# Kernel optimization log

Hardware: AMD Instinct MI355X
Metric: run time of the kernel (lower is better)

The kernel has to match this reference:

```python
import jax, jax.numpy as jnp
import numpy as np

B, N, T = 1, 4096, 512
WQ, HK = 32, 128
ATOM_S, ATOM_Z, TOKEN_S, TOKEN_Z = 128, 16, 384, 128
FEAT = 3 + 1 + 128 + 4 * 64  # 388


def _indexing_matrix(K, Wq, Hk):
    # faithful port of get_indexing_matrix: one-hot banded gather matrix [2K, K*h]
    h = Hk // (Wq // 2)
    ar = jnp.arange(2 * K)
    idx = jnp.clip(ar[None, :] - ar[:, None] + h // 2, 0, h + 1)
    idx = idx.reshape(K, 2, 2 * K)[:, 0, :]                 # [K, 2K]
    oh = jax.nn.one_hot(idx, h + 2, dtype=jnp.float32)[..., 1:-1]  # [K, 2K, h]
    return jnp.transpose(oh, (1, 0, 2)).reshape(2 * K, K * h)


def _to_keys(x, M, Wq, Hk):
    b, n, d = x.shape
    k = n // Wq
    x = x.reshape(b, 2 * k, Wq // 2, d)
    return jnp.einsum('bjid,jk->bkid', x, M).reshape(b, k, Hk, d)


def _ln(x, g, b, eps=1e-5):
    m = jnp.mean(x, axis=-1, keepdims=True)
    v = jnp.var(x, axis=-1, keepdims=True)
    return (x - m) * jax.lax.rsqrt(v + eps) * g + b


def setup_inputs() -> dict:
    key = jax.random.key(0)
    ks = jax.random.split(key, 24)
    s = 0.02
    tok_idx = jnp.sort(jax.random.randint(ks[0], (B, N), 0, T), axis=-1)
    return {
        'ref_pos': jax.random.normal(ks[1], (B, N, 3), jnp.float32),
        'ref_charge': jax.random.normal(ks[2], (B, N), jnp.float32),
        'ref_element': jax.random.uniform(ks[3], (B, N, 128), jnp.float32),
        'ref_atom_name_chars': jax.random.uniform(ks[4], (B, N, 4, 64), jnp.float32),
        'atom_pad_mask': jnp.ones((B, N), dtype=bool),
        'ref_space_uid': jnp.sort(jax.random.randint(ks[5], (B, N), 0, 512), axis=-1),
        'atom_to_token': jax.nn.one_hot(tok_idx, T, dtype=jnp.float32),
        's_trunk': jax.random.normal(ks[6], (B, T, TOKEN_S), jnp.float32),
        'z': jax.random.normal(ks[7], (B, T, T, TOKEN_Z), jnp.float32),
        # learned params, stored [in, out] so y = x @ W (+ b)
        'W_feat': jax.random.normal(ks[8], (FEAT, ATOM_S), jnp.float32) * s,
        'b_feat': jnp.zeros((ATOM_S,), jnp.float32),
        'W_pos': jax.random.normal(ks[9], (3, ATOM_Z), jnp.float32) * s,
        'W_dist': jax.random.normal(ks[10], (1, ATOM_Z), jnp.float32) * s,
        'W_mask': jax.random.normal(ks[11], (1, ATOM_Z), jnp.float32) * s,
        'ln_s_g': jnp.ones((TOKEN_S,), jnp.float32),
        'ln_s_b': jnp.zeros((TOKEN_S,), jnp.float32),
        'W_s2c': jax.random.normal(ks[12], (TOKEN_S, ATOM_S), jnp.float32) * s,
        'ln_z_g': jnp.ones((TOKEN_Z,), jnp.float32),
        'ln_z_b': jnp.zeros((TOKEN_Z,), jnp.float32),
        'W_z2p': jax.random.normal(ks[13], (TOKEN_Z, ATOM_Z), jnp.float32) * s,
        'W_cq': jax.random.normal(ks[14], (ATOM_S, ATOM_Z), jnp.float32) * s,
        'W_ck': jax.random.normal(ks[15], (ATOM_S, ATOM_Z), jnp.float32) * s,
        'W_m1': jax.random.normal(ks[16], (ATOM_Z, ATOM_Z), jnp.float32) * s,
        'W_m2': jax.random.normal(ks[17], (ATOM_Z, ATOM_Z), jnp.float32) * s,
        'W_m3': jax.random.normal(ks[18], (ATOM_Z, ATOM_Z), jnp.float32) * s,
    }


def reference(ref_pos, ref_charge, ref_element, ref_atom_name_chars, atom_pad_mask,
              ref_space_uid, atom_to_token, s_trunk, z,
              W_feat, b_feat, W_pos, W_dist, W_mask,
              ln_s_g, ln_s_b, W_s2c, ln_z_g, ln_z_b, W_z2p,
              W_cq, W_ck, W_m1, W_m2, W_m3):
    b, n, _ = ref_pos.shape
    k = n // WQ
    atom_feats = jnp.concatenate(
        [ref_pos, ref_charge[..., None], ref_element,
         ref_atom_name_chars.reshape(b, n, 4 * 64)], axis=-1)
    c = atom_feats @ W_feat + b_feat                       # [B,N,atom_s]
    q = c
    M = _indexing_matrix(k, WQ, HK)
    tk = lambda x: _to_keys(x, M, WQ, HK)

    pos_q = ref_pos.reshape(b, k, WQ, 1, 3)
    pos_k = tk(ref_pos).reshape(b, k, 1, HK, 3)
    d = pos_k - pos_q                                      # [B,K,W,H,3]
    d_norm = 1.0 / (1.0 + jnp.sum(d * d, axis=-1, keepdims=True))

    mq = atom_pad_mask.reshape(b, k, WQ, 1)
    mk = tk(atom_pad_mask[..., None].astype(jnp.float32)).reshape(b, k, 1, HK) > 0.5
    uq = ref_space_uid.reshape(b, k, WQ, 1)
    uk = tk(ref_space_uid[..., None].astype(jnp.float32)).reshape(b, k, 1, HK).astype(ref_space_uid.dtype)
    v = (mq & mk & (uq == uk)).astype(jnp.float32)[..., None]  # [B,K,W,H,1]

    p = (d @ W_pos) * v
    p = p + (d_norm @ W_dist) * v
    p = p + (v @ W_mask) * v

    # structure_prediction branch
    s2c = _ln(s_trunk, ln_s_g, ln_s_b) @ W_s2c             # [B,T,atom_s]
    c = c + jnp.einsum('bnt,btd->bnd', atom_to_token, s2c)
    a2t_q = atom_to_token.reshape(b, k, WQ, -1)            # [B,K,W,T]
    a2t_k = tk(atom_to_token)                              # [B,K,H,T]
    zp = _ln(z, ln_z_g, ln_z_b) @ W_z2p                    # [B,T,T,atom_z]
    tmp = jnp.einsum('bwki,bijd->bwkjd', a2t_q, zp)        # [B,K,W,T,atom_z]
    p = p + jnp.einsum('bwkjd,bwlj->bwkld', tmp, a2t_k)    # [B,K,W,H,atom_z]

    p = p + jax.nn.relu(c).reshape(b, k, WQ, 1, -1) @ W_cq
    p = p + jax.nn.relu(tk(c)).reshape(b, k, 1, HK, -1) @ W_ck

    h1 = jax.nn.relu(p) @ W_m1
    h2 = jax.nn.relu(h1) @ W_m2
    p = p + jax.nn.relu(h2) @ W_m3
    return (q, c, p)
```

## Files before the change

kernel.cpp:

```cpp
#include <hip/hip_runtime.h>

#define N_ATOMS 4096
#define T_TOK   512
#define TOKEN_S 384
#define TOKEN_Z 128

using bfrag = __attribute__((ext_vector_type(8))) short;
using f4    = __attribute__((ext_vector_type(4))) float;

__device__ __forceinline__ short f2bf(float f) {
    unsigned u = __float_as_uint(f);
    unsigned r = u + 0x7FFFu + ((u >> 16) & 1u);
    return (short)(r >> 16);
}
__device__ __forceinline__ float bf2f(unsigned short s) {
    return __uint_as_float(((unsigned)s) << 16);
}

__global__ __launch_bounds__(256) void setup_kernel(
    const float* __restrict__ a2t, const float* __restrict__ Wz,
    const float* __restrict__ gz, const float* __restrict__ bz,
    const float* __restrict__ Wf, const float* __restrict__ Wcq,
    const float* __restrict__ Wck, const float* __restrict__ Ws2c,
    const float* __restrict__ gs, const float* __restrict__ bs,
    int* __restrict__ tok, short* __restrict__ zpW,
    short* __restrict__ featW, short* __restrict__ WcqF,
    short* __restrict__ WckF, short* __restrict__ s2cW,
    float* __restrict__ bias16, float* __restrict__ cs16,
    float* __restrict__ cs128, float* __restrict__ bs128) {
    const int b = blockIdx.x, tid = threadIdx.x;
    if (b >= 53) {
        const int wave = tid >> 6, lane = tid & 63;
        const int n = (b - 53) * 4 + wave;
        const float* row = a2t + (size_t)n * T_TOK;
        int found = 0;
#pragma unroll
        for (int m = 0; m < T_TOK / 64; ++m)
            if (row[lane + 64 * m] > 0.5f) found = lane + 64 * m;
#pragma unroll
        for (int off = 32; off >= 1; off >>= 1)
            found = max(found, __shfl_xor(found, off, 64));
        if (lane == 0) tok[n] = found;
        return;
    }
    if (b == 51) {
        const int o = tid >> 3, s = tid & 7;
        const float* vec = (o < 16) ? bz : gz;
        const int n = o & 15;
        float p = 0.f;
#pragma unroll
        for (int i = 0; i < 16; ++i) {
            const int k = s + 8 * i;
            p += vec[k] * Wz[k * 16 + n];
        }
        p += __shfl_xor(p, 1, 64); p += __shfl_xor(p, 2, 64);
        p += __shfl_xor(p, 4, 64);
        if (s == 0) { if (o < 16) bias16[n] = p; else cs16[n] = p; }
        return;
    }
    if (b == 52) {
        const int o = tid & 127, arr = tid >> 7;
        const float* vec = arr ? bs : gs;
        float s = 0.f;
        for (int k = 0; k < TOKEN_S; ++k)
            s += vec[k] * Ws2c[(size_t)k * 128 + o];
        if (arr) bs128[o] = s; else cs128[o] = s;
        return;
    }
    const int id = b * 256 + tid;
    const int lane = id & 63, fs = id >> 6;
    const int quad = lane >> 4, n = lane & 15;
    short v[8];
    short* dst;
    if (fs < 4) {
#pragma unroll
        for (int j = 0; j < 8; ++j) {
            int k = fs * 32 + quad * 8 + j;
            v[j] = f2bf(gz[k] * Wz[k * 16 + n]);
        }
        dst = zpW + (size_t)(fs * 64 + lane) * 8;
    } else if (fs < 100) {
        const int idx = fs - 4, kb = idx >> 3, nt = idx & 7;
#pragma unroll
        for (int j = 0; j < 8; ++j) {
            int f = 4 + kb * 32 + quad * 8 + j;
            v[j] = f2bf(Wf[(size_t)f * 128 + nt * 16 + n]);
        }
        dst = featW + (size_t)(idx * 64 + lane) * 8;
    } else if (fs < 104) {
        const int kb = fs - 100;
#pragma unroll
        for (int j = 0; j < 8; ++j) {
            int k = kb * 32 + quad * 8 + j;
            v[j] = f2bf(Wcq[k * 16 + n]);
        }
        dst = WcqF + (size_t)(kb * 64 + lane) * 8;
    } else if (fs < 108) {
        const int kb = fs - 104;
#pragma unroll
        for (int j = 0; j < 8; ++j) {
            int k = kb * 32 + quad * 8 + j;
            v[j] = f2bf(Wck[k * 16 + n]);
        }
        dst = WckF + (size_t)(kb * 64 + lane) * 8;
    } else {
        const int idx = fs - 108, kb = idx >> 3, nt = idx & 7;
#pragma unroll
        for (int j = 0; j < 8; ++j) {
            int k = kb * 32 + quad * 8 + j;
            v[j] = f2bf(gs[k] * Ws2c[(size_t)k * 128 + nt * 16 + n]);
        }
        dst = s2cW + (size_t)(idx * 64 + lane) * 8;
    }
#pragma unroll
    for (int j = 0; j < 8; ++j) dst[j] = v[j];
}

__global__ __launch_bounds__(256) void s2c_mfma_kernel(
    const float* __restrict__ s_trunk, const short* __restrict__ s2cW,
    const float* __restrict__ cs128, const float* __restrict__ bs128,
    float* __restrict__ s2c) {
    const int wave = threadIdx.x >> 6, lane = threadIdx.x & 63;
    const int m = lane & 15, quad = lane >> 4;
    const int wg = blockIdx.x * 4 + wave;
    const int tile = wg >> 3, nt = wg & 7;
    const int t0 = tile * 16;
    const float* xrow = s_trunk + (size_t)(t0 + m) * TOKEN_S;

    bfrag A[12];
    float xs = 0.f, xq = 0.f;
#pragma unroll
    for (int kb = 0; kb < 12; ++kb) {
        const float4* p = (const float4*)(xrow + kb * 32 + quad * 8);
        float4 x0 = p[0], x1 = p[1];
        const float xv[8] = {x0.x, x0.y, x0.z, x0.w, x1.x, x1.y, x1.z, x1.w};
#pragma unroll
        for (int j = 0; j < 8; ++j) {
            A[kb][j] = f2bf(xv[j]);
            xs += xv[j]; xq = fmaf(xv[j], xv[j], xq);
        }
    }
    xs += __shfl_xor(xs, 16, 64); xs += __shfl_xor(xs, 32, 64);
    xq += __shfl_xor(xq, 16, 64); xq += __shfl_xor(xq, 32, 64);
    const float mean = xs * (1.f / TOKEN_S);
    const float var  = xq * (1.f / TOKEN_S) - mean * mean;
    const float rstd = rsqrtf(var + 1e-5f);
    const float mrs  = mean * rstd;

    const bfrag* Bb = (const bfrag*)s2cW;
    f4 acc = {0.f, 0.f, 0.f, 0.f};
#pragma unroll
    for (int kb = 0; kb < 12; ++kb)
        acc = __builtin_amdgcn_mfma_f32_16x16x32_bf16(
            A[kb], Bb[(kb * 8 + nt) * 64 + lane], acc, 0, 0, 0);

    const int cn = nt * 16 + m;
    const float csn = cs128[cn], bsn = bs128[cn];
#pragma unroll
    for (int reg = 0; reg < 4; ++reg) {
        const int r = quad * 4 + reg;
        const float rs = __shfl(rstd, r, 64);
        const float ms = __shfl(mrs, r, 64);
        s2c[(size_t)(t0 + r) * 128 + cn] = rs * acc[reg] - ms * csn + bsn;
    }
}

__global__ __launch_bounds__(256) void zp_mfma_kernel(
    const float* __restrict__ z, const short* __restrict__ zpW,
    const float* __restrict__ bias16, const float* __restrict__ cs16,
    unsigned short* __restrict__ zp_bf) {
    const int wave = threadIdx.x >> 6, lane = threadIdx.x & 63;
    const int m = lane & 15, quad = lane >> 4;
    const size_t r0 = ((size_t)blockIdx.x * 4 + wave) * 16;
    const float* zrow = z + (r0 + m) * (size_t)TOKEN_Z;

    bfrag A[4];
    float xs = 0.f, xq = 0.f;
#pragma unroll
    for (int kb = 0; kb < 4; ++kb) {
        const float4* p = (const float4*)(zrow + kb * 32 + quad * 8);
        float4 x0 = p[0], x1 = p[1];
        const float xv[8] = {x0.x, x0.y, x0.z, x0.w, x1.x, x1.y, x1.z, x1.w};
#pragma unroll
        for (int j = 0; j < 8; ++j) {
            A[kb][j] = f2bf(xv[j]);
            xs += xv[j]; xq = fmaf(xv[j], xv[j], xq);
        }
    }
    xs += __shfl_xor(xs, 16, 64); xs += __shfl_xor(xs, 32, 64);
    xq += __shfl_xor(xq, 16, 64); xq += __shfl_xor(xq, 32, 64);
    const float mean = xs * (1.f / TOKEN_Z);
    const float var  = xq * (1.f / TOKEN_Z) - mean * mean;
    const float rstd = rsqrtf(var + 1e-5f);
    const float mrs  = mean * rstd;

    const bfrag* wb = (const bfrag*)zpW;
    f4 acc = {0.f, 0.f, 0.f, 0.f};
#pragma unroll
    for (int kb = 0; kb < 4; ++kb)
        acc = __builtin_amdgcn_mfma_f32_16x16x32_bf16(A[kb], wb[kb * 64 + lane],
                                                      acc, 0, 0, 0);
    const float csn = cs16[m], bn = bias16[m];
#pragma unroll
    for (int reg = 0; reg < 4; ++reg) {
        const int r = quad * 4 + reg;
        const float rs = __shfl(rstd, r, 64);
        const float ms = __shfl(mrs, r, 64);
        zp_bf[(r0 + r) * 16 + m] =
            (unsigned short)f2bf(rs * acc[reg] - ms * csn + bn);
    }
}

__global__ __launch_bounds__(128) void featcatk_kernel(
    const float* __restrict__ pos, const float* __restrict__ charge,
    const float* __restrict__ elem, const float* __restrict__ namec,
    const float* __restrict__ Wf, const float* __restrict__ bf,
    const float* __restrict__ s2c, const int* __restrict__ tok,
    const short* __restrict__ featW, const short* __restrict__ WcqF,
    const short* __restrict__ WckF, float* __restrict__ q_out,
    float* __restrict__ c_out, float* __restrict__ acq,
    float* __restrict__ ack) {
    __shared__ short ctile[16 * 136];
    const int wave = threadIdx.x >> 6, lane = threadIdx.x & 63;
    const int m = lane & 15, quad = lane >> 4;
    const int a0 = blockIdx.x * 16;
    const int ntb = wave * 4;

    f4 acc[4];
#pragma unroll
    for (int nt = 0; nt < 4; ++nt) acc[nt] = (f4){0.f, 0.f, 0.f, 0.f};
    const bfrag* Bb = (const bfrag*)featW;
#pragma unroll
    for (int kb = 0; kb < 12; ++kb) {
        const int f0 = kb * 32 + quad * 8;
        const float* src = (kb < 4)
            ? (elem + (size_t)(a0 + m) * 128 + f0)
            : (namec + (size_t)(a0 + m) * 256 + f0 - 128);
        float4 x0 = ((const float4*)src)[0];
        float4 x1 = ((const float4*)src)[1];
        bfrag A;
        A[0] = f2bf(x0.x); A[1] = f2bf(x0.y); A[2] = f2bf(x0.z); A[3] = f2bf(x0.w);
        A[4] = f2bf(x1.x); A[5] = f2bf(x1.y); A[6] = f2bf(x1.z); A[7] = f2bf(x1.w);
#pragma unroll
        for (int nt = 0; nt < 4; ++nt)
            acc[nt] = __builtin_amdgcn_mfma_f32_16x16x32_bf16(
                A, Bb[(kb * 8 + ntb + nt) * 64 + lane], acc[nt], 0, 0, 0);
    }
    float px[4], py[4], pz[4], ch[4];
    int tk4[4];
#pragma unroll
    for (int reg = 0; reg < 4; ++reg) {
        const int a = a0 + quad * 4 + reg;
        px[reg] = pos[a * 3 + 0]; py[reg] = pos[a * 3 + 1];
        pz[reg] = pos[a * 3 + 2]; ch[reg] = charge[a];
        tk4[reg] = tok[a];
    }
#pragma unroll
    for (int nt = 0; nt < 4; ++nt) {
        const int cn = (ntb + nt) * 16 + m;
        const float w0 = Wf[cn], w1 = Wf[128 + cn], w2 = Wf[256 + cn],
                    w3 = Wf[384 + cn], bv = bf[cn];
#pragma unroll
        for (int reg = 0; reg < 4; ++reg) {
            const int r = quad * 4 + reg;
            float qv = acc[nt][reg] + px[reg] * w0 + py[reg] * w1 +
                       pz[reg] * w2 + ch[reg] * w3 + bv;
            q_out[(size_t)(a0 + r) * 128 + cn] = qv;
            float cv = qv + s2c[(size_t)tk4[reg] * 128 + cn];
            c_out[(size_t)(a0 + r) * 128 + cn] = cv;
            ctile[r * 136 + cn] = f2bf(fmaxf(cv, 0.f));
        }
    }
    __syncthreads();
    const bfrag* BW = wave ? (const bfrag*)WckF : (const bfrag*)WcqF;
    float* dst = wave ? ack : acq;
    f4 a2 = {0.f, 0.f, 0.f, 0.f};
#pragma unroll
    for (int kb = 0; kb < 4; ++kb) {
        bfrag Af = *(const bfrag*)&ctile[m * 136 + kb * 32 + quad * 8];
        a2 = __builtin_amdgcn_mfma_f32_16x16x32_bf16(Af, BW[kb * 64 + lane],
                                                     a2, 0, 0, 0);
    }
#pragma unroll
    for (int reg = 0; reg < 4; ++reg)
        dst[(size_t)(a0 + quad * 4 + reg) * 16 + m] = a2[reg];
}

__global__ __launch_bounds__(256) void pair_mfma_kernel(
    const float* __restrict__ pos, const int* __restrict__ uid,
    const int* __restrict__ tok, const unsigned short* __restrict__ zp_bf,
    const float* __restrict__ acq, const float* __restrict__ ack,
    const float* __restrict__ W_pos, const float* __restrict__ W_dist,
    const float* __restrict__ W_mask, const float* __restrict__ W_m1,
    const float* __restrict__ W_m2, const float* __restrict__ W_m3,
    float* __restrict__ p_out) {
    const int wave = threadIdx.x >> 6, lane = threadIdx.x & 63;
    const int m = lane & 15, quad = lane >> 4;
    const int qa = blockIdx.x * 4 + wave;
    const int j = qa >> 5;

    bfrag A1, A2, A3;
#pragma unroll
    for (int jj = 0; jj < 4; ++jj) {
        const int d = quad * 4 + jj;
        A1[jj] = f2bf(W_m1[d * 16 + m]); A1[jj + 4] = 0;
        A2[jj] = f2bf(W_m2[d * 16 + m]); A2[jj + 4] = 0;
        A3[jj] = f2bf(W_m3[d * 16 + m]); A3[jj + 4] = 0;
    }
    float wp0[4], wp1[4], wp2[4], wd[4], wm[4];
#pragma unroll
    for (int jj = 0; jj < 4; ++jj) {
        const int d = quad * 4 + jj;
        wp0[jj] = W_pos[d]; wp1[jj] = W_pos[16 + d]; wp2[jj] = W_pos[32 + d];
        wd[jj] = W_dist[d]; wm[jj] = W_mask[d];
    }
    const float pqx = pos[qa * 3 + 0], pqy = pos[qa * 3 + 1],
                pqz = pos[qa * 3 + 2];
    const int uq = uid[qa], tq = tok[qa];
    const float4 aq = *(const float4*)(acq + (size_t)qa * 16 + quad * 4);
    const float aqv[4] = {aq.x, aq.y, aq.z, aq.w};
    float* pbase = p_out + (size_t)qa * 2048;

    const f4 zero = {0.f, 0.f, 0.f, 0.f};
#pragma unroll
    for (int g = 0; g < 8; ++g) {
        const int kk = g * 16 + m;
        const int src = j * 32 + kk - 48;
        const bool valid = ((unsigned)src < (unsigned)N_ATOMS);
        float dx = 0.f, dy = 0.f, dz = 0.f, dn = 0.f, vflag = 0.f;
        float zv[4] = {0.f, 0.f, 0.f, 0.f}, av[4] = {0.f, 0.f, 0.f, 0.f};
        if (valid) {
            dx = pos[src * 3 + 0] - pqx;
            dy = pos[src * 3 + 1] - pqy;
            dz = pos[src * 3 + 2] - pqz;
            dn = 1.f / (1.f + dx * dx + dy * dy + dz * dz);
            vflag = (uid[src] == uq) ? 1.f : 0.f;
            const int tk_ = tok[src];
            ushort4 zl = *(const ushort4*)(zp_bf +
                            ((size_t)tq * 512 + tk_) * 16 + quad * 4);
            float4 al = *(const float4*)(ack + (size_t)src * 16 + quad * 4);
            zv[0] = bf2f(zl.x); zv[1] = bf2f(zl.y);
            zv[2] = bf2f(zl.z); zv[3] = bf2f(zl.w);
            av[0] = al.x; av[1] = al.y; av[2] = al.z; av[3] = al.w;
        }
        float pb[4];
        bfrag B;
#pragma unroll
        for (int jj = 0; jj < 4; ++jj) {
            float t = dx * wp0[jj] + dy * wp1[jj] + dz * wp2[jj] +
                      dn * wd[jj] + wm[jj];
            pb[jj] = vflag * t + zv[jj] + av[jj] + aqv[jj];
            B[jj] = f2bf(fmaxf(pb[jj], 0.f));
            B[jj + 4] = 0;
        }
        f4 t1 = __builtin_amdgcn_mfma_f32_16x16x32_bf16(A1, B, zero, 0, 0, 0);
        bfrag B2;
#pragma unroll
        for (int jj = 0; jj < 4; ++jj) {
            B2[jj] = f2bf(fmaxf(t1[jj], 0.f)); B2[jj + 4] = 0;
        }
        f4 t2 = __builtin_amdgcn_mfma_f32_16x16x32_bf16(A2, B2, zero, 0, 0, 0);
        bfrag B3;
#pragma unroll
        for (int jj = 0; jj < 4; ++jj) {
            B3[jj] = f2bf(fmaxf(t2[jj], 0.f)); B3[jj + 4] = 0;
        }
        f4 t3 = __builtin_amdgcn_mfma_f32_16x16x32_bf16(A3, B3, zero, 0, 0, 0);
        float4 o = make_float4(pb[0] + t3[0], pb[1] + t3[1],
                               pb[2] + t3[2], pb[3] + t3[3]);
        *(float4*)(pbase + kk * 16 + quad * 4) = o;
    }
}

extern "C" void kernel_launch(void* const* d_in, const int* in_sizes, int n_in,
                              void* d_out, int out_size, void* d_ws, size_t ws_size,
                              hipStream_t stream) {
    const float* ref_pos     = (const float*)d_in[0];
    const float* ref_charge  = (const float*)d_in[1];
    const float* ref_element = (const float*)d_in[2];
    const float* ref_name    = (const float*)d_in[3];
    const int*   uid         = (const int*)d_in[5];
    const float* a2t         = (const float*)d_in[6];
    const float* s_trunk     = (const float*)d_in[7];
    const float* z           = (const float*)d_in[8];
    const float* W_feat      = (const float*)d_in[9];
    const float* b_feat      = (const float*)d_in[10];
    const float* W_pos       = (const float*)d_in[11];
    const float* W_dist      = (const float*)d_in[12];
    const float* W_mask      = (const float*)d_in[13];
    const float* ln_s_g      = (const float*)d_in[14];
    const float* ln_s_b      = (const float*)d_in[15];
    const float* W_s2c       = (const float*)d_in[16];
    const float* ln_z_g      = (const float*)d_in[17];
    const float* ln_z_b      = (const float*)d_in[18];
    const float* W_z2p       = (const float*)d_in[19];
    const float* W_cq        = (const float*)d_in[20];
    const float* W_ck        = (const float*)d_in[21];
    const float* W_m1        = (const float*)d_in[22];
    const float* W_m2        = (const float*)d_in[23];
    const float* W_m3        = (const float*)d_in[24];

    float* out = (float*)d_out;
    float* q_out = out;
    float* c_out = out + 524288;
    float* p_out = out + 1048576;

    char* w = (char*)d_ws;
    unsigned short* zp_bf = (unsigned short*)w;
    float* s2c  = (float*)(w + 8388608);
    float* acq  = s2c + 65536;
    float* ack  = acq + 65536;
    int*   tok  = (int*)(ack + 65536);
    short* zpW   = (short*)(tok + 4096);
    short* featW = zpW + 2048;
    short* WcqF  = featW + 49152;
    short* WckF  = WcqF + 2048;
    short* s2cW  = WckF + 2048;
    float* bias16 = (float*)(s2cW + 49152);
    float* cs16   = bias16 + 16;
    float* cs128  = cs16 + 16;
    float* bs128  = cs128 + 128;

    setup_kernel<<<1077, 256, 0, stream>>>(a2t, W_z2p, ln_z_g, ln_z_b,
                                           W_feat, W_cq, W_ck, W_s2c,
                                           ln_s_g, ln_s_b, tok, zpW, featW,
                                           WcqF, WckF, s2cW, bias16, cs16,
                                           cs128, bs128);
    s2c_mfma_kernel<<<64, 256, 0, stream>>>(s_trunk, s2cW, cs128, bs128, s2c);
    zp_mfma_kernel<<<4096, 256, 0, stream>>>(z, zpW, bias16, cs16, zp_bf);
    featcatk_kernel<<<256, 128, 0, stream>>>(ref_pos, ref_charge, ref_element,
                                             ref_name, W_feat, b_feat, s2c, tok,
                                             featW, WcqF, WckF,
                                             q_out, c_out, acq, ack);
    pair_mfma_kernel<<<1024, 256, 0, stream>>>(ref_pos, uid, tok, zp_bf,
                                               acq, ack, W_pos, W_dist, W_mask,
                                               W_m1, W_m2, W_m3, p_out);
}
```

Before: 293.3 us.

## Compute zp projection only for token pairs reachable within atom window band

Builds per-query-token bounds on the key tokens its atoms can attend to (window of ±79 atoms), turns them into a worklist of 16-token tiles, and runs the z layernorm+projection only over those tiles instead of all 512x512 token pairs. This cuts most of the reading of the 128 MB z tensor. It relies on atom_to_token being sorted so the band is contiguous, and it adds small extra kernels and atomics.

```diff
diff --git a/kernel.cpp b/kernel.cpp
--- a/kernel.cpp
+++ b/kernel.cpp
@@ -27,7 +27,8 @@
     short* __restrict__ featW, short* __restrict__ WcqF,
     short* __restrict__ WckF, short* __restrict__ s2cW,
     float* __restrict__ bias16, float* __restrict__ cs16,
-    float* __restrict__ cs128, float* __restrict__ bs128) {
+    float* __restrict__ cs128, float* __restrict__ bs128,
+    int* __restrict__ lo, int* __restrict__ hi) {
     const int b = blockIdx.x, tid = threadIdx.x;
     if (b >= 53) {
         const int wave = tid >> 6, lane = tid & 63;
@@ -59,6 +60,8 @@
         return;
     }
     if (b == 52) {
+        lo[tid] = 0x7FFFFFFF; lo[tid + 256] = 0x7FFFFFFF;
+        hi[tid] = -1;         hi[tid + 256] = -1;
         const int o = tid & 127, arr = tid >> 7;
         const float* vec = arr ? bs : gs;
         float s = 0.f;
@@ -114,6 +117,40 @@
     }
 #pragma unroll
     for (int j = 0; j < 8; ++j) dst[j] = v[j];
+}
+
+__global__ __launch_bounds__(256) void band_kernel(
+    const int* __restrict__ tok, int* __restrict__ lo, int* __restrict__ hi) {
+    const int a = blockIdx.x * 256 + threadIdx.x;
+    const int t = tok[a];
+    int am = a - 79; if (am < 0) am = 0;
+    int ap = a + 79; if (ap > N_ATOMS - 1) ap = N_ATOMS - 1;
+    atomicMin(&lo[t], tok[am]);
+    atomicMax(&hi[t], tok[ap]);
+}
+
+__global__ __launch_bounds__(512) void worklist_kernel(
+    const int* __restrict__ lo, const int* __restrict__ hi,
+    int* __restrict__ wl, int* __restrict__ wl_count) {
+    __shared__ int scan[512];
+    const int t = threadIdx.x;
+    const int l = lo[t], h = hi[t];
+    const int n = (h >= l) ? ((h - l) >> 4) + 1 : 0;
+    scan[t] = n;
+    __syncthreads();
+    for (int off = 1; off < 512; off <<= 1) {
+        int add = (t >= off) ? scan[t - off] : 0;
+        __syncthreads();
+        scan[t] += add;
+        __syncthreads();
+    }
+    const int off0 = scan[t] - n;
+    for (int i = 0; i < n; ++i) {
+        int tk0 = l + i * 16;
+        if (tk0 > T_TOK - 16) tk0 = T_TOK - 16;
+        wl[off0 + i] = (t << 16) | tk0;
+    }
+    if (t == 511) *wl_count = scan[511];
 }
 
 __global__ __launch_bounds__(256) void s2c_mfma_kernel(
@@ -165,49 +202,58 @@
     }
 }
 
-__global__ __launch_bounds__(256) void zp_mfma_kernel(
+__global__ __launch_bounds__(256) void zp_wl_kernel(
     const float* __restrict__ z, const short* __restrict__ zpW,
     const float* __restrict__ bias16, const float* __restrict__ cs16,
+    const int* __restrict__ wl, const int* __restrict__ wl_count,
     unsigned short* __restrict__ zp_bf) {
     const int wave = threadIdx.x >> 6, lane = threadIdx.x & 63;
     const int m = lane & 15, quad = lane >> 4;
-    const size_t r0 = ((size_t)blockIdx.x * 4 + wave) * 16;
-    const float* zrow = z + (r0 + m) * (size_t)TOKEN_Z;
-
-    bfrag A[4];
-    float xs = 0.f, xq = 0.f;
-#pragma unroll
-    for (int kb = 0; kb < 4; ++kb) {
-        const float4* p = (const float4*)(zrow + kb * 32 + quad * 8);
-        float4 x0 = p[0], x1 = p[1];
-        const float xv[8] = {x0.x, x0.y, x0.z, x0.w, x1.x, x1.y, x1.z, x1.w};
-#pragma unroll
-        for (int j = 0; j < 8; ++j) {
-            A[kb][j] = f2bf(xv[j]);
-            xs += xv[j]; xq = fmaf(xv[j], xv[j], xq);
-        }
-    }
-    xs += __shfl_xor(xs, 16, 64); xs += __shfl_xor(xs, 32, 64);
-    xq += __shfl_xor(xq, 16, 64); xq += __shfl_xor(xq, 32, 64);
-    const float mean = xs * (1.f / TOKEN_Z);
-    const float var  = xq * (1.f / TOKEN_Z) - mean * mean;
-    const float rstd = rsqrtf(var + 1e-5f);
-    const float mrs  = mean * rstd;
-
+    const int nwaves = gridDim.x * 4;
+    const int count = *wl_count;
     const bfrag* wb = (const bfrag*)zpW;
-    f4 acc = {0.f, 0.f, 0.f, 0.f};
-#pragma unroll
-    for (int kb = 0; kb < 4; ++kb)
-        acc = __builtin_amdgcn_mfma_f32_16x16x32_bf16(A[kb], wb[kb * 64 + lane],
-                                                      acc, 0, 0, 0);
     const float csn = cs16[m], bn = bias16[m];
-#pragma unroll
-    for (int reg = 0; reg < 4; ++reg) {
-        const int r = quad * 4 + reg;
-        const float rs = __shfl(rstd, r, 64);
-        const float ms = __shfl(mrs, r, 64);
-        zp_bf[(r0 + r) * 16 + m] =
-            (unsigned short)f2bf(rs * acc[reg] - ms * csn + bn);
+
+    for (int idx = blockIdx.x * 4 + wave; idx < count; idx += nwaves) {
+        const int e = wl[idx];
+        const int tq = e >> 16, tk0 = e & 0xFFFF;
+        const size_t r0 = (size_t)tq * T_TOK + tk0;
+        const float* zrow = z + (r0 + m) * (size_t)TOKEN_Z;
+
+        bfrag A[4];
+        float xs = 0.f, xq = 0.f;
+#pragma unroll
+        for (int kb = 0; kb < 4; ++kb) {
+            const float4* p = (const float4*)(zrow + kb * 32 + quad * 8);
+            float4 x0 = p[0], x1 = p[1];
+            const float xv[8] = {x0.x, x0.y, x0.z, x0.w,
+                                 x1.x, x1.y, x1.z, x1.w};
+#pragma unroll
+            for (int j = 0; j < 8; ++j) {
+                A[kb][j] = f2bf(xv[j]);
+                xs += xv[j]; xq = fmaf(xv[j], xv[j], xq);
+            }
+        }
+        xs += __shfl_xor(xs, 16, 64); xs += __shfl_xor(xs, 32, 64);
+        xq += __shfl_xor(xq, 16, 64); xq += __shfl_xor(xq, 32, 64);
+        const float mean = xs * (1.f / TOKEN_Z);
+        const float var  = xq * (1.f / TOKEN_Z) - mean * mean;
+        const float rstd = rsqrtf(var + 1e-5f);
+        const float mrs  = mean * rstd;
+
+        f4 acc = {0.f, 0.f, 0.f, 0.f};
+#pragma unroll
+        for (int kb = 0; kb < 4; ++kb)
+            acc = __builtin_amdgcn_mfma_f32_16x16x32_bf16(
+                A[kb], wb[kb * 64 + lane], acc, 0, 0, 0);
+#pragma unroll
+        for (int reg = 0; reg < 4; ++reg) {
+            const int r = quad * 4 + reg;
+            const float rs = __shfl(rstd, r, 64);
+            const float ms = __shfl(mrs, r, 64);
+            zp_bf[(r0 + r) * 16 + m] =
+                (unsigned short)f2bf(rs * acc[reg] - ms * csn + bn);
+        }
     }
 }
 
@@ -337,7 +383,7 @@
             vflag = (uid[src] == uq) ? 1.f : 0.f;
             const int tk_ = tok[src];
             ushort4 zl = *(const ushort4*)(zp_bf +
-                            ((size_t)tq * 512 + tk_) * 16 + quad * 4);
+                            ((size_t)tq * T_TOK + tk_) * 16 + quad * 4);
             float4 al = *(const float4*)(ack + (size_t)src * 16 + quad * 4);
             zv[0] = bf2f(zl.x); zv[1] = bf2f(zl.y);
             zv[2] = bf2f(zl.z); zv[3] = bf2f(zl.w);
@@ -420,14 +466,21 @@
     float* cs16   = bias16 + 16;
     float* cs128  = cs16 + 16;
     float* bs128  = cs128 + 128;
+    int*   lo     = (int*)(bs128 + 128);
+    int*   hi     = lo + 512;
+    int*   wl     = hi + 512;
+    int*   wl_cnt = wl + 16448;
 
     setup_kernel<<<1077, 256, 0, stream>>>(a2t, W_z2p, ln_z_g, ln_z_b,
                                            W_feat, W_cq, W_ck, W_s2c,
                                            ln_s_g, ln_s_b, tok, zpW, featW,
                                            WcqF, WckF, s2cW, bias16, cs16,
-                                           cs128, bs128);
+                                           cs128, bs128, lo, hi);
+    band_kernel<<<16, 256, 0, stream>>>(tok, lo, hi);
+    worklist_kernel<<<1, 512, 0, stream>>>(lo, hi, wl, wl_cnt);
     s2c_mfma_kernel<<<64, 256, 0, stream>>>(s_trunk, s2cW, cs128, bs128, s2c);
-    zp_mfma_kernel<<<4096, 256, 0, stream>>>(z, zpW, bias16, cs16, zp_bf);
+    zp_wl_kernel<<<512, 256, 0, stream>>>(z, zpW, bias16, cs16, wl, wl_cnt,
+                                          zp_bf);
     featcatk_kernel<<<256, 128, 0, stream>>>(ref_pos, ref_charge, ref_element,
                                              ref_name, W_feat, b_feat, s2c, tok,
                                              featW, WcqF, WckF,
```

Result: faster. 273.7 us (-6.7%).
